# Performance work log

Hardware: AMD Instinct MI355X
Metric: run time of the kernel (lower is better)

The kernel has to match this reference:

```python
import jax, jax.numpy as jnp
import numpy as np

B, S, D, H = 1, 2048, 1024, 16
DH = D // H  # 64
ROPE_THETA = 10000.0


def _rope_tables(seq_len, half_dim, theta):
    inv = 1.0 / (theta ** (np.arange(0, half_dim, dtype=np.float32) / half_dim))
    ang = np.arange(seq_len, dtype=np.float32)[:, None] * inv[None, :]
    return jnp.asarray(np.cos(ang)), jnp.asarray(np.sin(ang))


def setup_inputs() -> dict:
    key = jax.random.key(0)
    ks = jax.random.split(key, 6)
    x = jax.random.normal(ks[0], (B, S, D), dtype=jnp.float32)
    # block-diagonal mask over ~4 packed images -> sorted segment ids
    seg_ids = jnp.sort(jax.random.randint(ks[1], (S,), 0, 4, dtype=jnp.int32))
    freqs_cos, freqs_sin = _rope_tables(S, DH // 2, ROPE_THETA)
    scale = 1.0 / np.sqrt(D)
    wq = jax.random.normal(ks[2], (D, D), dtype=jnp.float32) * scale
    wk = jax.random.normal(ks[3], (D, D), dtype=jnp.float32) * scale
    wv = jax.random.normal(ks[4], (D, D), dtype=jnp.float32) * scale
    wo = jax.random.normal(ks[5], (D, D), dtype=jnp.float32) * scale
    return {"x": x, "seg_ids": seg_ids, "freqs_cos": freqs_cos,
            "freqs_sin": freqs_sin, "wq": wq, "wk": wk, "wv": wv, "wo": wo}


def _apply_rope(t, cos, sin):
    # t: [B,S,H,DH]; interpret last dim as DH//2 complex pairs (real, imag)
    tr = t.reshape(B, S, H, DH // 2, 2)
    a, b = tr[..., 0], tr[..., 1]
    c = cos[None, :, None, :]  # [1,S,1,DH/2]
    s = sin[None, :, None, :]
    out = jnp.stack([a * c - b * s, a * s + b * c], axis=-1)
    return out.reshape(B, S, H, DH)


def reference(x, seg_ids, freqs_cos, freqs_sin, wq, wk, wv, wo):
    q = (x @ wq.T).reshape(B, S, H, DH)
    k = (x @ wk.T).reshape(B, S, H, DH)
    v = (x @ wv.T).reshape(B, S, H, DH)
    q = _apply_rope(q, freqs_cos, freqs_sin)
    k = _apply_rope(k, freqs_cos, freqs_sin)
    scores = jnp.einsum('bqhd,bkhd->bhqk', q, k) / np.float32(np.sqrt(DH))
    block_mask = (seg_ids[:, None] == seg_ids[None, :])  # [S,S] block-diagonal
    scores = jnp.where(block_mask[None, None], scores, jnp.float32(-1e9))
    attn = jax.nn.softmax(scores, axis=-1)
    out = jnp.einsum('bhqk,bkhd->bqhd', attn, v).reshape(B, S, D)
    return out @ wo.T
```

## Files before the change

### kernel.cpp

```cpp
#include <hip/hip_runtime.h>

typedef __bf16 bf16;
typedef __bf16 bf16x4 __attribute__((ext_vector_type(4)));
typedef __bf16 bf16x8 __attribute__((ext_vector_type(8)));
typedef float  f32x4  __attribute__((ext_vector_type(4)));

#define S_LEN 2048
#define D_DIM 1024
#define NHEAD 16
#define DHEAD 64

__device__ __forceinline__ void async_cp16(const bf16* g, bf16* l) {
  __builtin_amdgcn_global_load_lds(
      (__attribute__((address_space(1))) void*)(void*)g,
      (__attribute__((address_space(3))) void*)l,
      16, 0, 0);
}

__global__ __launch_bounds__(256) void cvt_k(
    const float* __restrict__ x,  const float* __restrict__ w0,
    const float* __restrict__ w1, const float* __restrict__ w2,
    const float* __restrict__ w3, bf16* __restrict__ dst)
{
  int i = blockIdx.x * 256 + threadIdx.x;
  const float* src;
  int off;
  if (i < (1 << 18)) {
    src = x; off = i;
  } else {
    int j = i - (1 << 18);
    int s = j >> 17;
    off = j & ((1 << 17) - 1);
    src = (s == 0) ? w0 : (s == 1) ? w1 : (s == 2) ? w2 : w3;
  }
  f32x4 a = *(const f32x4*)(src + (size_t)off * 8);
  f32x4 b = *(const f32x4*)(src + (size_t)off * 8 + 4);
  bf16x8 o;
  o[0] = (bf16)a[0]; o[1] = (bf16)a[1]; o[2] = (bf16)a[2]; o[3] = (bf16)a[3];
  o[4] = (bf16)b[0]; o[5] = (bf16)b[1]; o[6] = (bf16)b[2]; o[7] = (bf16)b[3];
  *((bf16x8*)dst + i) = o;
}

__global__ __launch_bounds__(256) void gemm_qkv(
    const bf16* __restrict__ A,
    const bf16* __restrict__ B0, const bf16* __restrict__ B1,
    const bf16* __restrict__ B2,
    const float* __restrict__ cosT, const float* __restrict__ sinT,
    bf16* __restrict__ Cbase)
{
  constexpr int K = 1024, N = 1024;
  const int z = blockIdx.z;
  const bf16* W = (z == 0) ? B0 : (z == 1) ? B1 : B2;
  bf16* C = Cbase + (size_t)z * 2048 * 1024;

  __shared__ bf16 As0[128 * 32] __attribute__((aligned(16)));
  __shared__ bf16 As1[128 * 32] __attribute__((aligned(16)));
  __shared__ bf16 Bs0[64 * 32] __attribute__((aligned(16)));
  __shared__ bf16 Bs1[64 * 32] __attribute__((aligned(16)));

  const int t = threadIdx.x;
  const int lane = t & 63;
  const int w = t >> 6;
  const int lm = lane & 15, lq = lane >> 4;
  const int wr = w >> 1, wc = w & 1;
  const int bm = blockIdx.y, bn = blockIdx.x;

  const bf16* Abase = A + (size_t)bm * 128 * K;
  const bf16* Wbase = W + (size_t)bn * 64 * K;

  f32x4 acc[4][2] = {};

  for (int kk = 0; kk < K; kk += 64) {
#pragma unroll
    for (int g = 0; g < 2; ++g) {
      int c = (w * 2 + g) * 64 + lane;
      int row = c >> 2, k8 = c & 3;
      const bf16* ga = Abase + (size_t)row * K + kk + k8 * 8;
      async_cp16(ga, As0 + (w * 2 + g) * 512);
      async_cp16(ga + 32, As1 + (w * 2 + g) * 512);
    }
    {
      int c = w * 64 + lane;
      int row = c >> 2, k8 = c & 3;
      const bf16* gb = Wbase + (size_t)row * K + kk + k8 * 8;
      async_cp16(gb, Bs0 + w * 512);
      async_cp16(gb + 32, Bs1 + w * 512);
    }
    __syncthreads();

#pragma unroll
    for (int ks = 0; ks < 2; ++ks) {
      const bf16* As = ks ? As1 : As0;
      const bf16* Bs = ks ? Bs1 : Bs0;
      bf16x8 af[4], bfr[2];
#pragma unroll
      for (int mi = 0; mi < 4; ++mi)
        af[mi] = *(const bf16x8*)&As[(wr * 64 + mi * 16 + lm) * 32 + lq * 8];
#pragma unroll
      for (int ni = 0; ni < 2; ++ni)
        bfr[ni] = *(const bf16x8*)&Bs[(wc * 32 + ni * 16 + lm) * 32 + lq * 8];
#pragma unroll
      for (int mi = 0; mi < 4; ++mi)
#pragma unroll
        for (int ni = 0; ni < 2; ++ni)
          acc[mi][ni] = __builtin_amdgcn_mfma_f32_16x16x32_bf16(
              af[mi], bfr[ni], acc[mi][ni], 0, 0, 0);
    }
    __syncthreads();
  }

  if (z < 2) {
    const float scale = (z == 0) ? 0.125f : 1.0f;
#pragma unroll
    for (int mi = 0; mi < 4; ++mi)
#pragma unroll
      for (int ni = 0; ni < 2; ++ni) {
        int gcol = bn * 64 + wc * 32 + ni * 16 + lm;
        int p = (gcol & 63) >> 1;
        bool even = (gcol & 1) == 0;
#pragma unroll
        for (int r = 0; r < 4; ++r) {
          int row = bm * 128 + wr * 64 + mi * 16 + lq * 4 + r;
          float v = acc[mi][ni][r];
          float mate = __shfl_xor(v, 1);
          float cv = cosT[row * 32 + p];
          float sv = sinT[row * 32 + p];
          float res = even ? (v * cv - mate * sv) : (mate * sv + v * cv);
          C[(size_t)row * N + gcol] = (bf16)(res * scale);
        }
      }
  } else {
#pragma unroll
    for (int mi = 0; mi < 4; ++mi)
#pragma unroll
      for (int ni = 0; ni < 2; ++ni) {
        int gcol = bn * 64 + wc * 32 + ni * 16 + lm;
#pragma unroll
        for (int r = 0; r < 4; ++r) {
          int row = bm * 128 + wr * 64 + mi * 16 + lq * 4 + r;
          C[(size_t)row * N + gcol] = (bf16)acc[mi][ni][r];
        }
      }
  }
}

__global__ __launch_bounds__(256) void gemm_wo(
    const bf16* __restrict__ A, const bf16* __restrict__ W,
    float* __restrict__ C)
{
  constexpr int K = 1024, N = 1024;
  const int z = blockIdx.z;

  __shared__ bf16 As0[128 * 32] __attribute__((aligned(16)));
  __shared__ bf16 As1[128 * 32] __attribute__((aligned(16)));
  __shared__ bf16 Bs0[64 * 32] __attribute__((aligned(16)));
  __shared__ bf16 Bs1[64 * 32] __attribute__((aligned(16)));

  const int t = threadIdx.x;
  const int lane = t & 63;
  const int w = t >> 6;
  const int lm = lane & 15, lq = lane >> 4;
  const int wr = w >> 1, wc = w & 1;
  const int bm = blockIdx.y, bn = blockIdx.x;

  const bf16* Abase = A + (size_t)bm * 128 * K;
  const bf16* Wbase = W + (size_t)bn * 64 * K;

  f32x4 acc[4][2] = {};

  for (int kk = z * 512; kk < z * 512 + 512; kk += 64) {
#pragma unroll
    for (int g = 0; g < 2; ++g) {
      int c = (w * 2 + g) * 64 + lane;
      int row = c >> 2, k8 = c & 3;
      const bf16* ga = Abase + (size_t)row * K + kk + k8 * 8;
      async_cp16(ga, As0 + (w * 2 + g) * 512);
      async_cp16(ga + 32, As1 + (w * 2 + g) * 512);
    }
    {
      int c = w * 64 + lane;
      int row = c >> 2, k8 = c & 3;
      const bf16* gb = Wbase + (size_t)row * K + kk + k8 * 8;
      async_cp16(gb, Bs0 + w * 512);
      async_cp16(gb + 32, Bs1 + w * 512);
    }
    __syncthreads();

#pragma unroll
    for (int ks = 0; ks < 2; ++ks) {
      const bf16* As = ks ? As1 : As0;
      const bf16* Bs = ks ? Bs1 : Bs0;
      bf16x8 af[4], bfr[2];
#pragma unroll
      for (int mi = 0; mi < 4; ++mi)
        af[mi] = *(const bf16x8*)&As[(wr * 64 + mi * 16 + lm) * 32 + lq * 8];
#pragma unroll
      for (int ni = 0; ni < 2; ++ni)
        bfr[ni] = *(const bf16x8*)&Bs[(wc * 32 + ni * 16 + lm) * 32 + lq * 8];
#pragma unroll
      for (int mi = 0; mi < 4; ++mi)
#pragma unroll
        for (int ni = 0; ni < 2; ++ni)
          acc[mi][ni] = __builtin_amdgcn_mfma_f32_16x16x32_bf16(
              af[mi], bfr[ni], acc[mi][ni], 0, 0, 0);
    }
    __syncthreads();
  }

#pragma unroll
  for (int mi = 0; mi < 4; ++mi)
#pragma unroll
    for (int ni = 0; ni < 2; ++ni) {
      int col = bn * 64 + wc * 32 + ni * 16 + lm;
#pragma unroll
      for (int r = 0; r < 4; ++r) {
        int row = bm * 128 + wr * 64 + mi * 16 + lq * 4 + r;
        atomicAdd(&C[(size_t)row * N + col], acc[mi][ni][r]);
      }
    }
}

__global__ __launch_bounds__(256) void prep_k(
    const bf16* __restrict__ v, bf16* __restrict__ vt,
    const int* __restrict__ seg, int* __restrict__ kbr)
{
  __shared__ bf16 tile[64 * 65];
  __shared__ int firstv[4];
  const int b = blockIdx.x;
  const int t = threadIdx.x;

  if (b < 512) {
    const int s0t = (b & 31) * 64;
    const int d0t = (b >> 5) * 64;
    const int c = t & 63, r0 = t >> 6;
#pragma unroll
    for (int r = r0; r < 64; r += 4)
      tile[r * 65 + c] = v[(size_t)(s0t + r) * D_DIM + d0t + c];
    __syncthreads();
#pragma unroll
    for (int r = r0; r < 64; r += 4)
      vt[(size_t)(d0t + r) * S_LEN + s0t + c] = tile[c * 65 + r];
  } else {
    if (t < 4) firstv[t] = S_LEN;
    __syncthreads();
    for (int i = t; i < S_LEN; i += 256) {
      int s = seg[i];
      if (i == 0 || seg[i - 1] != s) atomicMin(&firstv[s], i);
    }
    __syncthreads();
    if (t < 32) {
      int smin = seg[t * 64], smax = seg[t * 64 + 63];
      int lb = S_LEN, ub = S_LEN;
      for (int vv = smin; vv < 4; ++vv) lb = min(lb, firstv[vv]);
      for (int vv = smax + 1; vv < 4; ++vv) ub = min(ub, firstv[vv]);
      kbr[t * 2] = lb >> 6;
      kbr[t * 2 + 1] = (ub - 1) >> 6;
    }
  }
}

__global__ __launch_bounds__(256) void attn_k(
    const bf16* __restrict__ Q, const bf16* __restrict__ Kmat,
    const bf16* __restrict__ Vt, const int* __restrict__ seg,
    const int* __restrict__ kbr,
    float* __restrict__ Opar, float* __restrict__ Lpar)
{
  __shared__ bf16 Ks[64 * 72] __attribute__((aligned(16)));
  __shared__ bf16 Vs[64 * 72] __attribute__((aligned(16)));
  __shared__ bf16 Ps[4][16 * 72] __attribute__((aligned(16)));
  __shared__ int segk[64];

  const int h = blockIdx.y;
  const int qt = blockIdx.x & 31, par = blockIdx.x >> 5;
  const int q0 = qt * 64;
  const int t = threadIdx.x, lane = t & 63, w = t >> 6;
  const int lm = lane & 15, lq = lane >> 4;
  const int qrow = q0 + w * 16;

  const int kb0f = kbr[qt * 2], kb1f = kbr[qt * 2 + 1];

  bf16x8 qf[2];
#pragma unroll
  for (int ks = 0; ks < 2; ++ks)
    qf[ks] = *(const bf16x8*)(Q + (size_t)(qrow + lm) * D_DIM + h * DHEAD +
                              ks * 32 + lq * 8);

  int sq[4];
  float l_i[4];
#pragma unroll
  for (int r = 0; r < 4; ++r) {
    sq[r] = seg[qrow + lq * 4 + r];
    l_i[r] = 0.0f;
  }
  f32x4 o[4] = {};

  const int srow0 = t >> 3, sch = (t & 7) * 8;
  const int srow1 = (256 + t) >> 3;

  const int kbS = kb0f + par;
  f32x4 pk0, pk1, pv0, pv1;
  int psg;
  if (kbS <= kb1f) {
    const int k0 = kbS * 64;
    pk0 = *(const f32x4*)(Kmat + (size_t)(k0 + srow0) * D_DIM + h * DHEAD + sch);
    pk1 = *(const f32x4*)(Kmat + (size_t)(k0 + srow1) * D_DIM + h * DHEAD + sch);
    pv0 = *(const f32x4*)(Vt + (size_t)(h * DHEAD + srow0) * S_LEN + k0 + sch);
    pv1 = *(const f32x4*)(Vt + (size_t)(h * DHEAD + srow1) * S_LEN + k0 + sch);
    if (t < 64) psg = seg[k0 + t];
  }

  for (int kb = kbS; kb <= kb1f; kb += 2) {
    __syncthreads();
    *(f32x4*)&Ks[srow0 * 72 + sch] = pk0;
    *(f32x4*)&Ks[srow1 * 72 + sch] = pk1;
    *(f32x4*)&Vs[srow0 * 72 + sch] = pv0;
    *(f32x4*)&Vs[srow1 * 72 + sch] = pv1;
    if (t < 64) segk[t] = psg;
    __syncthreads();

    if (kb + 2 <= kb1f) {
      const int k0 = (kb + 2) * 64;
      pk0 = *(const f32x4*)(Kmat + (size_t)(k0 + srow0) * D_DIM + h * DHEAD + sch);
      pk1 = *(const f32x4*)(Kmat + (size_t)(k0 + srow1) * D_DIM + h * DHEAD + sch);
      pv0 = *(const f32x4*)(Vt + (size_t)(h * DHEAD + srow0) * S_LEN + k0 + sch);
      pv1 = *(const f32x4*)(Vt + (size_t)(h * DHEAD + srow1) * S_LEN + k0 + sch);
      if (t < 64) psg = seg[k0 + t];
    }

    f32x4 sa[4] = {};
#pragma unroll
    for (int ks = 0; ks < 2; ++ks) {
      bf16x8 kf[4];
#pragma unroll
      for (int ni = 0; ni < 4; ++ni)
        kf[ni] = *(const bf16x8*)&Ks[(ni * 16 + lm) * 72 + ks * 32 + lq * 8];
#pragma unroll
      for (int ni = 0; ni < 4; ++ni)
        sa[ni] = __builtin_amdgcn_mfma_f32_16x16x32_bf16(qf[ks], kf[ni],
                                                         sa[ni], 0, 0, 0);
    }

    int sk[4];
#pragma unroll
    for (int ni = 0; ni < 4; ++ni) sk[ni] = segk[ni * 16 + lm];

#pragma unroll
    for (int r = 0; r < 4; ++r)
#pragma unroll
      for (int ni = 0; ni < 4; ++ni) {
        float p = (sq[r] == sk[ni]) ? __expf(sa[ni][r]) : 0.0f;
        l_i[r] += p;
        Ps[w][(lq * 4 + r) * 72 + ni * 16 + lm] = (bf16)p;
      }

#pragma unroll
    for (int ks = 0; ks < 2; ++ks) {
      bf16x8 pf = *(const bf16x8*)&Ps[w][lm * 72 + ks * 32 + lq * 8];
      bf16x8 vf[4];
#pragma unroll
      for (int ni = 0; ni < 4; ++ni)
        vf[ni] = *(const bf16x8*)&Vs[(ni * 16 + lm) * 72 + ks * 32 + lq * 8];
#pragma unroll
      for (int ni = 0; ni < 4; ++ni)
        o[ni] = __builtin_amdgcn_mfma_f32_16x16x32_bf16(pf, vf[ni], o[ni],
                                                        0, 0, 0);
    }
  }

  float* Ob = Opar + ((size_t)(par * NHEAD + h) * S_LEN) * DHEAD;
  float* Lb = Lpar + (size_t)(par * NHEAD + h) * S_LEN;
#pragma unroll
  for (int r = 0; r < 4; ++r) {
    float l = l_i[r];
    l += __shfl_xor(l, 1);
    l += __shfl_xor(l, 2);
    l += __shfl_xor(l, 4);
    l += __shfl_xor(l, 8);
    int row = qrow + lq * 4 + r;
    if (lm == 0) Lb[row] = l;
#pragma unroll
    for (int ni = 0; ni < 4; ++ni)
      Ob[(size_t)row * DHEAD + ni * 16 + lm] = o[ni][r];
  }
}

__global__ __launch_bounds__(256) void combine_k(
    const float* __restrict__ Opar, const float* __restrict__ Lpar,
    bf16* __restrict__ AO)
{
  int idx = blockIdx.x * 256 + threadIdx.x;
  int c4 = idx & 15;
  int rh = idx >> 4;
  int row = rh & 2047;
  int h = rh >> 11;
  const size_t PO = (size_t)NHEAD * S_LEN * DHEAD;
  const float* o0 = Opar + ((size_t)h * S_LEN + row) * DHEAD + c4 * 4;
  f32x4 a = *(const f32x4*)o0;
  f32x4 b = *(const f32x4*)(o0 + PO);
  float l = Lpar[(size_t)h * S_LEN + row] +
            Lpar[(size_t)NHEAD * S_LEN + (size_t)h * S_LEN + row];
  float inv = 1.0f / l;
  bf16x4 ov;
#pragma unroll
  for (int j = 0; j < 4; ++j) ov[j] = (bf16)((a[j] + b[j]) * inv);
  *(bf16x4*)(AO + (size_t)row * D_DIM + h * DHEAD + c4 * 4) = ov;
}

extern "C" void kernel_launch(void* const* d_in, const int* in_sizes, int n_in,
                              void* d_out, int out_size, void* d_ws,
                              size_t ws_size, hipStream_t stream)
{
  const float* x  = (const float*)d_in[0];
  const int*   sg = (const int*)d_in[1];
  const float* fc = (const float*)d_in[2];
  const float* fs = (const float*)d_in[3];
  const float* wq = (const float*)d_in[4];
  const float* wk = (const float*)d_in[5];
  const float* wv = (const float*)d_in[6];
  const float* wo = (const float*)d_in[7];
  float* out = (float*)d_out;

  const size_t MAT = (size_t)S_LEN * D_DIM;
  const size_t WSZ = (size_t)D_DIM * D_DIM;
  bf16* xb  = (bf16*)d_ws;
  bf16* wqb = xb + MAT;
  bf16* wkb = wqb + WSZ;
  bf16* wvb = wkb + WSZ;
  bf16* wob = wvb + WSZ;
  bf16* q0  = wob + WSZ;
  bf16* k0  = q0 + MAT;
  bf16* v0  = k0 + MAT;
  bf16* vt  = v0 + MAT;
  bf16* ao  = vt + MAT;
  float* opar = (float*)(ao + MAT);
  float* lpar = opar + 2 * MAT;
  int*   kbr  = (int*)(lpar + 2 * NHEAD * S_LEN);

  dim3 blk(256);
  hipMemsetAsync(out, 0, (size_t)out_size * sizeof(float), stream);
  cvt_k<<<dim3(3072), blk, 0, stream>>>(x, wq, wk, wv, wo, xb);
  gemm_qkv<<<dim3(16, 16, 3), blk, 0, stream>>>(xb, wqb, wkb, wvb, fc, fs, q0);
  prep_k<<<dim3(513), blk, 0, stream>>>(v0, vt, sg, kbr);
  attn_k<<<dim3(64, 16), blk, 0, stream>>>(q0, k0, vt, sg, kbr, opar, lpar);
  combine_k<<<dim3(2048), blk, 0, stream>>>(opar, lpar, ao);
  gemm_wo<<<dim3(16, 16, 2), blk, 0, stream>>>(ao, wob, out);
}
```

Measured before the change: 160.2 us.

## Fuse V transpose into QKV GEMM epilogue, fold segment prep, drop split-K atomics

The QKV GEMM's V path now writes its output directly in transposed layout as packed bf16x4 stores. This removes the separate prep_k transpose kernel and the V staging buffer. The segment-boundary computation moves into an extra block of the conversion kernel. The output projection GEMM switches from split-K with atomicAdd (plus a memset) to a 64x64 tile grid with plain stores, which removes the atomics, the memset and a launch at the cost of smaller per-block tiles.

```diff
diff --git a/kernel.cpp b/kernel.cpp
--- a/kernel.cpp
+++ b/kernel.cpp
@@ -20,25 +20,48 @@
 __global__ __launch_bounds__(256) void cvt_k(
     const float* __restrict__ x,  const float* __restrict__ w0,
     const float* __restrict__ w1, const float* __restrict__ w2,
-    const float* __restrict__ w3, bf16* __restrict__ dst)
-{
-  int i = blockIdx.x * 256 + threadIdx.x;
-  const float* src;
-  int off;
-  if (i < (1 << 18)) {
-    src = x; off = i;
+    const float* __restrict__ w3, bf16* __restrict__ dst,
+    const int* __restrict__ seg, int* __restrict__ kbr)
+{
+  __shared__ int firstv[4];
+  const int b = blockIdx.x;
+  const int t = threadIdx.x;
+
+  if (b < 3072) {
+    int i = b * 256 + t;
+    const float* src;
+    int off;
+    if (i < (1 << 18)) {
+      src = x; off = i;
+    } else {
+      int j = i - (1 << 18);
+      int s = j >> 17;
+      off = j & ((1 << 17) - 1);
+      src = (s == 0) ? w0 : (s == 1) ? w1 : (s == 2) ? w2 : w3;
+    }
+    f32x4 a = *(const f32x4*)(src + (size_t)off * 8);
+    f32x4 bb = *(const f32x4*)(src + (size_t)off * 8 + 4);
+    bf16x8 o;
+    o[0] = (bf16)a[0];  o[1] = (bf16)a[1];  o[2] = (bf16)a[2];  o[3] = (bf16)a[3];
+    o[4] = (bf16)bb[0]; o[5] = (bf16)bb[1]; o[6] = (bf16)bb[2]; o[7] = (bf16)bb[3];
+    *((bf16x8*)dst + i) = o;
   } else {
-    int j = i - (1 << 18);
-    int s = j >> 17;
-    off = j & ((1 << 17) - 1);
-    src = (s == 0) ? w0 : (s == 1) ? w1 : (s == 2) ? w2 : w3;
-  }
-  f32x4 a = *(const f32x4*)(src + (size_t)off * 8);
-  f32x4 b = *(const f32x4*)(src + (size_t)off * 8 + 4);
-  bf16x8 o;
-  o[0] = (bf16)a[0]; o[1] = (bf16)a[1]; o[2] = (bf16)a[2]; o[3] = (bf16)a[3];
-  o[4] = (bf16)b[0]; o[5] = (bf16)b[1]; o[6] = (bf16)b[2]; o[7] = (bf16)b[3];
-  *((bf16x8*)dst + i) = o;
+    if (t < 4) firstv[t] = S_LEN;
+    __syncthreads();
+    for (int i = t; i < S_LEN; i += 256) {
+      int s = seg[i];
+      if (i == 0 || seg[i - 1] != s) atomicMin(&firstv[s], i);
+    }
+    __syncthreads();
+    if (t < 32) {
+      int smin = seg[t * 64], smax = seg[t * 64 + 63];
+      int lb = S_LEN, ub = S_LEN;
+      for (int vv = smin; vv < 4; ++vv) lb = min(lb, firstv[vv]);
+      for (int vv = smax + 1; vv < 4; ++vv) ub = min(ub, firstv[vv]);
+      kbr[t * 2] = lb >> 6;
+      kbr[t * 2 + 1] = (ub - 1) >> 6;
+    }
+  }
 }
 
 __global__ __launch_bounds__(256) void gemm_qkv(
@@ -46,7 +69,7 @@
     const bf16* __restrict__ B0, const bf16* __restrict__ B1,
     const bf16* __restrict__ B2,
     const float* __restrict__ cosT, const float* __restrict__ sinT,
-    bf16* __restrict__ Cbase)
+    bf16* __restrict__ Cbase, bf16* __restrict__ Vt)
 {
   constexpr int K = 1024, N = 1024;
   const int z = blockIdx.z;
@@ -135,11 +158,11 @@
 #pragma unroll
       for (int ni = 0; ni < 2; ++ni) {
         int gcol = bn * 64 + wc * 32 + ni * 16 + lm;
-#pragma unroll
-        for (int r = 0; r < 4; ++r) {
-          int row = bm * 128 + wr * 64 + mi * 16 + lq * 4 + r;
-          C[(size_t)row * N + gcol] = (bf16)acc[mi][ni][r];
-        }
+        int rowb = bm * 128 + wr * 64 + mi * 16 + lq * 4;
+        bf16x4 pack;
+#pragma unroll
+        for (int r = 0; r < 4; ++r) pack[r] = (bf16)acc[mi][ni][r];
+        *(bf16x4*)(Vt + (size_t)gcol * S_LEN + rowb) = pack;
       }
   }
 }
@@ -149,10 +172,9 @@
     float* __restrict__ C)
 {
   constexpr int K = 1024, N = 1024;
-  const int z = blockIdx.z;
-
-  __shared__ bf16 As0[128 * 32] __attribute__((aligned(16)));
-  __shared__ bf16 As1[128 * 32] __attribute__((aligned(16)));
+
+  __shared__ bf16 As0[64 * 32] __attribute__((aligned(16)));
+  __shared__ bf16 As1[64 * 32] __attribute__((aligned(16)));
   __shared__ bf16 Bs0[64 * 32] __attribute__((aligned(16)));
   __shared__ bf16 Bs1[64 * 32] __attribute__((aligned(16)));
 
@@ -160,26 +182,20 @@
   const int lane = t & 63;
   const int w = t >> 6;
   const int lm = lane & 15, lq = lane >> 4;
-  const int wr = w >> 1, wc = w & 1;
-  const int bm = blockIdx.y, bn = blockIdx.x;
-
-  const bf16* Abase = A + (size_t)bm * 128 * K;
+  const int bn = blockIdx.x, bm = blockIdx.y;
+
+  const bf16* Abase = A + (size_t)bm * 64 * K;
   const bf16* Wbase = W + (size_t)bn * 64 * K;
 
-  f32x4 acc[4][2] = {};
-
-  for (int kk = z * 512; kk < z * 512 + 512; kk += 64) {
-#pragma unroll
-    for (int g = 0; g < 2; ++g) {
-      int c = (w * 2 + g) * 64 + lane;
-      int row = c >> 2, k8 = c & 3;
-      const bf16* ga = Abase + (size_t)row * K + kk + k8 * 8;
-      async_cp16(ga, As0 + (w * 2 + g) * 512);
-      async_cp16(ga + 32, As1 + (w * 2 + g) * 512);
-    }
+  f32x4 acc[4] = {};
+
+  for (int kk = 0; kk < K; kk += 64) {
     {
       int c = w * 64 + lane;
       int row = c >> 2, k8 = c & 3;
+      const bf16* ga = Abase + (size_t)row * K + kk + k8 * 8;
+      async_cp16(ga, As0 + w * 512);
+      async_cp16(ga + 32, As1 + w * 512);
       const bf16* gb = Wbase + (size_t)row * K + kk + k8 * 8;
       async_cp16(gb, Bs0 + w * 512);
       async_cp16(gb + 32, Bs1 + w * 512);
@@ -190,71 +206,26 @@
     for (int ks = 0; ks < 2; ++ks) {
       const bf16* As = ks ? As1 : As0;
       const bf16* Bs = ks ? Bs1 : Bs0;
-      bf16x8 af[4], bfr[2];
-#pragma unroll
-      for (int mi = 0; mi < 4; ++mi)
-        af[mi] = *(const bf16x8*)&As[(wr * 64 + mi * 16 + lm) * 32 + lq * 8];
-#pragma unroll
-      for (int ni = 0; ni < 2; ++ni)
-        bfr[ni] = *(const bf16x8*)&Bs[(wc * 32 + ni * 16 + lm) * 32 + lq * 8];
-#pragma unroll
-      for (int mi = 0; mi < 4; ++mi)
-#pragma unroll
-        for (int ni = 0; ni < 2; ++ni)
-          acc[mi][ni] = __builtin_amdgcn_mfma_f32_16x16x32_bf16(
-              af[mi], bfr[ni], acc[mi][ni], 0, 0, 0);
-    }
-    __syncthreads();
-  }
-
-#pragma unroll
-  for (int mi = 0; mi < 4; ++mi)
-#pragma unroll
-    for (int ni = 0; ni < 2; ++ni) {
-      int col = bn * 64 + wc * 32 + ni * 16 + lm;
-#pragma unroll
-      for (int r = 0; r < 4; ++r) {
-        int row = bm * 128 + wr * 64 + mi * 16 + lq * 4 + r;
-        atomicAdd(&C[(size_t)row * N + col], acc[mi][ni][r]);
-      }
-    }
-}
-
-__global__ __launch_bounds__(256) void prep_k(
-    const bf16* __restrict__ v, bf16* __restrict__ vt,
-    const int* __restrict__ seg, int* __restrict__ kbr)
-{
-  __shared__ bf16 tile[64 * 65];
-  __shared__ int firstv[4];
-  const int b = blockIdx.x;
-  const int t = threadIdx.x;
-
-  if (b < 512) {
-    const int s0t = (b & 31) * 64;
-    const int d0t = (b >> 5) * 64;
-    const int c = t & 63, r0 = t >> 6;
-#pragma unroll
-    for (int r = r0; r < 64; r += 4)
-      tile[r * 65 + c] = v[(size_t)(s0t + r) * D_DIM + d0t + c];
-    __syncthreads();
-#pragma unroll
-    for (int r = r0; r < 64; r += 4)
-      vt[(size_t)(d0t + r) * S_LEN + s0t + c] = tile[c * 65 + r];
-  } else {
-    if (t < 4) firstv[t] = S_LEN;
-    __syncthreads();
-    for (int i = t; i < S_LEN; i += 256) {
-      int s = seg[i];
-      if (i == 0 || seg[i - 1] != s) atomicMin(&firstv[s], i);
-    }
-    __syncthreads();
-    if (t < 32) {
-      int smin = seg[t * 64], smax = seg[t * 64 + 63];
-      int lb = S_LEN, ub = S_LEN;
-      for (int vv = smin; vv < 4; ++vv) lb = min(lb, firstv[vv]);
-      for (int vv = smax + 1; vv < 4; ++vv) ub = min(ub, firstv[vv]);
-      kbr[t * 2] = lb >> 6;
-      kbr[t * 2 + 1] = (ub - 1) >> 6;
+      bf16x8 af = *(const bf16x8*)&As[(w * 16 + lm) * 32 + lq * 8];
+      bf16x8 bfr[4];
+#pragma unroll
+      for (int ni = 0; ni < 4; ++ni)
+        bfr[ni] = *(const bf16x8*)&Bs[(ni * 16 + lm) * 32 + lq * 8];
+#pragma unroll
+      for (int ni = 0; ni < 4; ++ni)
+        acc[ni] = __builtin_amdgcn_mfma_f32_16x16x32_bf16(
+            af, bfr[ni], acc[ni], 0, 0, 0);
+    }
+    __syncthreads();
+  }
+
+#pragma unroll
+  for (int ni = 0; ni < 4; ++ni) {
+    int col = bn * 64 + ni * 16 + lm;
+#pragma unroll
+    for (int r = 0; r < 4; ++r) {
+      int row = bm * 64 + w * 16 + lq * 4 + r;
+      C[(size_t)row * N + col] = acc[ni][r];
     }
   }
 }
@@ -429,19 +400,17 @@
   bf16* wob = wvb + WSZ;
   bf16* q0  = wob + WSZ;
   bf16* k0  = q0 + MAT;
-  bf16* v0  = k0 + MAT;
-  bf16* vt  = v0 + MAT;
+  bf16* vt  = k0 + MAT;
   bf16* ao  = vt + MAT;
   float* opar = (float*)(ao + MAT);
   float* lpar = opar + 2 * MAT;
   int*   kbr  = (int*)(lpar + 2 * NHEAD * S_LEN);
 
   dim3 blk(256);
-  hipMemsetAsync(out, 0, (size_t)out_size * sizeof(float), stream);
-  cvt_k<<<dim3(3072), blk, 0, stream>>>(x, wq, wk, wv, wo, xb);
-  gemm_qkv<<<dim3(16, 16, 3), blk, 0, stream>>>(xb, wqb, wkb, wvb, fc, fs, q0);
-  prep_k<<<dim3(513), blk, 0, stream>>>(v0, vt, sg, kbr);
+  cvt_k<<<dim3(3073), blk, 0, stream>>>(x, wq, wk, wv, wo, xb, sg, kbr);
+  gemm_qkv<<<dim3(16, 16, 3), blk, 0, stream>>>(xb, wqb, wkb, wvb, fc, fs,
+                                                q0, vt);
   attn_k<<<dim3(64, 16), blk, 0, stream>>>(q0, k0, vt, sg, kbr, opar, lpar);
   combine_k<<<dim3(2048), blk, 0, stream>>>(opar, lpar, ao);
-  gemm_wo<<<dim3(16, 16, 2), blk, 0, stream>>>(ao, wob, out);
-}
+  gemm_wo<<<dim3(16, 32), blk, 0, stream>>>(ao, wob, out);
+}
```

Result: faster. 148.8 us (-7.1%).
